# Performance work log

Hardware: AMD Instinct MI355X
Metric: run time of the kernel (lower is better)

The kernel has to match this reference:

```python
import jax, jax.numpy as jnp
import numpy as np

N_QUBITS = 4
DIM = 16  # 2**N_QUBITS
BATCH = 2_097_152


def _pauli_sign_tables():
    # Wire 0 is the most-significant bit in pennylane default.qubit ordering.
    bits = (np.arange(DIM)[:, None] >> np.arange(N_QUBITS - 1, -1, -1)[None, :]) & 1
    z_signs = (1 - 2 * bits).astype(np.float32)  # [16, 4], <Z_i> signs per basis state
    pairs = [(i, j) for i in range(N_QUBITS) for j in range(i + 1, N_QUBITS)]
    zz_signs = np.stack([z_signs[:, i] * z_signs[:, j] for i, j in pairs], axis=1)  # [16, 6]
    return jnp.asarray(z_signs), jnp.asarray(zz_signs)

Z_SIGNS, ZZ_SIGNS = _pauli_sign_tables()


def setup_inputs() -> dict:
    key = jax.random.key(0)
    ks = jax.random.split(key, 6)
    return {
        "x": jax.random.normal(ks[0], (BATCH, DIM), jnp.float32),
        "u_weights": jax.random.normal(ks[1], (N_QUBITS, 2), jnp.float32),
        "w1": jax.random.normal(ks[2], (16, 10), jnp.float32) * 0.3,
        "b1": jnp.zeros((16,), jnp.float32),
        "w2": jax.random.normal(ks[3], (2, 16), jnp.float32) * 0.25,
        "b2": jnp.zeros((2,), jnp.float32),
    }


def _circuit_features(x, u_weights):
    # StatePrep with normalize=True
    state = x / jnp.linalg.norm(x, axis=1, keepdims=True)
    state = state.astype(jnp.complex64).reshape(-1, 2, 2, 2, 2)  # [B, q0, q1, q2, q3]
    half_th = 0.5 * u_weights[:, 0]
    half_ph = 0.5 * u_weights[:, 1]
    c, s = jnp.cos(half_th), jnp.sin(half_th)
    for q in range(N_QUBITS):
        ry = jnp.stack([jnp.stack([c[q], -s[q]]),
                        jnp.stack([s[q], c[q]])]).astype(jnp.complex64)
        e = jnp.exp(-1j * half_ph[q].astype(jnp.complex64))
        rz = jnp.diag(jnp.stack([e, jnp.conj(e)]))
        u = rz @ ry  # RZ(phi) after RY(theta), single fused 2x2 gate
        state = jnp.moveaxis(state, q + 1, -1)
        state = state @ u.T  # new[a] = sum_b u[a,b] * old[b]
        state = jnp.moveaxis(state, -1, q + 1)
    probs = jnp.abs(state.reshape(-1, DIM)) ** 2  # [B, 16]
    z = probs @ Z_SIGNS    # [B, 4]  <Z_i>
    zz = probs @ ZZ_SIGNS  # [B, 6]  <Z_i Z_j>, i<j
    return jnp.concatenate([z, zz], axis=1)  # [B, 10]


def reference(x, u_weights, w1, b1, w2, b2):
    feats = _circuit_features(x, u_weights)
    h = jax.nn.relu(feats @ w1.T + b1)
    return h @ w2.T + b2  # [B, 2]
```

## Files before the change

### kernel.cpp

```cpp
#include <hip/hip_runtime.h>
#include <math.h>


#define PAD 20

__global__ __launch_bounds__(256) void qc_fused(
    const float* __restrict__ x, const float* __restrict__ uw,
    const float* __restrict__ w1, const float* __restrict__ b1,
    const float* __restrict__ w2, const float* __restrict__ b2,
    float* __restrict__ out, long batch)
{
    __shared__ float sX[256 * PAD];
    __shared__ float sCS[8];

    const int t = threadIdx.x;
    if (t < 8) {
        int q = t & 3;
        float th = 0.5f * uw[2 * q];
        sCS[t] = (t < 4) ? cosf(th) : sinf(th);
    }

    const float4* __restrict__ xv4 = (const float4*)x;
    const long nv4 = (long)batch * 4;
    const long base4 = (long)blockIdx.x * 1024;
    if (base4 + 1024 <= nv4) {
#pragma unroll
        for (int r = 0; r < 4; ++r) {
            int f = t + 256 * r;
            float4 v = xv4[base4 + f];
            ((float4*)(sX + (f >> 2) * PAD))[f & 3] = v;
        }
    } else {
#pragma unroll
        for (int r = 0; r < 4; ++r) {
            int f = t + 256 * r;
            long g = base4 + f;
            float4 v = (g < nv4) ? xv4[g] : make_float4(1.f, 0.f, 0.f, 0.f);
            ((float4*)(sX + (f >> 2) * PAD))[f & 3] = v;
        }
    }
    __syncthreads();

    const float* myx = sX + t * PAD;
    float y[16];
#pragma unroll
    for (int i = 0; i < 4; ++i) {
        float4 v = ((const float4*)myx)[i];
        y[4 * i + 0] = v.x; y[4 * i + 1] = v.y;
        y[4 * i + 2] = v.z; y[4 * i + 3] = v.w;
    }

    float cs[4], sn[4];
#pragma unroll
    for (int q = 0; q < 4; ++q) { cs[q] = sCS[q]; sn[q] = sCS[4 + q]; }

#pragma unroll
    for (int q = 0; q < 4; ++q) {
        const int st = 8 >> q;
#pragma unroll
        for (int i = 0; i < 16; ++i) {
            if ((i & st) == 0) {
                float a = y[i], b = y[i + st];
                y[i]      = fmaf(cs[q], a, -sn[q] * b);
                y[i + st] = fmaf(sn[q], a,  cs[q] * b);
            }
        }
    }

    float p[16];
#pragma unroll
    for (int i = 0; i < 16; ++i) p[i] = y[i] * y[i];
#pragma unroll
    for (int st = 1; st < 16; st <<= 1) {
#pragma unroll
        for (int i = 0; i < 16; ++i) {
            if ((i & st) == 0) {
                float a = p[i], b = p[i + st];
                p[i]      = a + b;
                p[i + st] = a - b;
            }
        }
    }

    const float rn = 1.0f / p[0];

    constexpr int bmap[10] = {8, 4, 2, 1, 12, 10, 9, 6, 5, 3};

    float tacc[16];
#pragma unroll
    for (int j = 0; j < 16; ++j) tacc[j] = 0.f;
#pragma unroll
    for (int f = 0; f < 10; ++f) {
        const float pf = p[bmap[f]];
#pragma unroll
        for (int j = 0; j < 16; ++j)
            tacc[j] = fmaf(w1[j * 10 + f], pf, tacc[j]);
    }

    float o0 = b2[0], o1 = b2[1];
#pragma unroll
    for (int j = 0; j < 16; ++j) {
        float h = fmaxf(fmaf(tacc[j], rn, b1[j]), 0.f);
        o0 = fmaf(w2[j],      h, o0);
        o1 = fmaf(w2[16 + j], h, o1);
    }

    const long sidx = (long)blockIdx.x * 256 + t;
    if (sidx < batch) ((float2*)out)[sidx] = make_float2(o0, o1);
}

extern "C" void kernel_launch(void* const* d_in, const int* in_sizes, int n_in,
                              void* d_out, int out_size, void* d_ws, size_t ws_size,
                              hipStream_t stream) {
    const float* x  = (const float*)d_in[0];
    const float* uw = (const float*)d_in[1];
    const float* w1 = (const float*)d_in[2];
    const float* b1 = (const float*)d_in[3];
    const float* w2 = (const float*)d_in[4];
    const float* b2 = (const float*)d_in[5];
    float* out = (float*)d_out;

    long batch = (long)(in_sizes[0] / 16);
    long blocks = (batch + 255) / 256;
    hipLaunchKernelGGL(qc_fused, dim3((unsigned)blocks), dim3(256), 0, stream,
                       x, uw, w1, b1, w2, b2, out, batch);
}
```

Measured before the change: 204.4 us.

## Persistent grid with double-buffered async global-to-LDS loads and XOR swizzle

Turns the kernel into a persistent grid-stride loop capped at 1280 blocks. The next 256-row tile is prefetched into a second LDS buffer with global_load_lds (direct global-to-LDS) while the current tile is computed. Padding is replaced by an XOR swizzle to avoid bank conflicts, and the trig coefficients are computed per thread and made uniform with readfirstlane. The aim is to overlap memory latency with compute on a bandwidth-bound kernel. The costs are a barrier per tile and reliance on builtin async-load semantics (synchronisation relies on __syncthreads waiting on vmcnt). Out-of-range rows now load row 0 instead of a unit vector, though their outputs are never stored.

After: 208.8 us. +2.1%, slower.

```diff
diff --git a/kernel.cpp b/kernel.cpp
--- a/kernel.cpp
+++ b/kernel.cpp
@@ -2,111 +2,124 @@
 #include <math.h>
 
 
-#define PAD 20
+#define TPB 256
 
-__global__ __launch_bounds__(256) void qc_fused(
+__device__ __forceinline__ void async_ld16(const float4* g, float4* l) {
+    __builtin_amdgcn_global_load_lds(
+        (const __attribute__((address_space(1))) void*)g,
+        (__attribute__((address_space(3))) void*)l,
+        16 , 0 , 0 );
+}
+
+__global__ __launch_bounds__(TPB) void qc_fused(
     const float* __restrict__ x, const float* __restrict__ uw,
     const float* __restrict__ w1, const float* __restrict__ b1,
     const float* __restrict__ w2, const float* __restrict__ b2,
     float* __restrict__ out, long batch)
 {
-    __shared__ float sX[256 * PAD];
-    __shared__ float sCS[8];
+    __shared__ float4 sX[2][1024];
 
     const int t = threadIdx.x;
-    if (t < 8) {
-        int q = t & 3;
-        float th = 0.5f * uw[2 * q];
-        sCS[t] = (t < 4) ? cosf(th) : sinf(th);
-    }
-
+    const long ntiles = (batch + TPB - 1) >> 8;
+    const long nv4 = batch * 4;
     const float4* __restrict__ xv4 = (const float4*)x;
-    const long nv4 = (long)batch * 4;
-    const long base4 = (long)blockIdx.x * 1024;
-    if (base4 + 1024 <= nv4) {
-#pragma unroll
-        for (int r = 0; r < 4; ++r) {
-            int f = t + 256 * r;
-            float4 v = xv4[base4 + f];
-            ((float4*)(sX + (f >> 2) * PAD))[f & 3] = v;
-        }
-    } else {
-#pragma unroll
-        for (int r = 0; r < 4; ++r) {
-            int f = t + 256 * r;
-            long g = base4 + f;
-            float4 v = (g < nv4) ? xv4[g] : make_float4(1.f, 0.f, 0.f, 0.f);
-            ((float4*)(sX + (f >> 2) * PAD))[f & 3] = v;
-        }
-    }
-    __syncthreads();
-
-    const float* myx = sX + t * PAD;
-    float y[16];
-#pragma unroll
-    for (int i = 0; i < 4; ++i) {
-        float4 v = ((const float4*)myx)[i];
-        y[4 * i + 0] = v.x; y[4 * i + 1] = v.y;
-        y[4 * i + 2] = v.z; y[4 * i + 3] = v.w;
-    }
 
     float cs[4], sn[4];
 #pragma unroll
-    for (int q = 0; q < 4; ++q) { cs[q] = sCS[q]; sn[q] = sCS[4 + q]; }
+    for (int q = 0; q < 4; ++q) {
+        float th = 0.5f * uw[2 * q];
+        cs[q] = __uint_as_float(__builtin_amdgcn_readfirstlane(__float_as_uint(cosf(th))));
+        sn[q] = __uint_as_float(__builtin_amdgcn_readfirstlane(__float_as_uint(sinf(th))));
+    }
+
+    auto stage = [&](long base4, float4* dst) {
+#pragma unroll
+        for (int r = 0; r < 4; ++r) {
+            int n = (r << 8) + t;
+            int gsw = (n & ~3) | ((n & 3) ^ ((n >> 3) & 3));
+            long g = base4 + gsw;
+            g = (g < nv4) ? g : 0;
+            async_ld16(xv4 + g, dst + n);
+        }
+    };
+
+    long tile = blockIdx.x;
+    int cur = 0;
+    if (tile < ntiles) stage(tile << 10, &sX[0][0]);
+    __syncthreads();
+
+    const int pq = (t >> 1) & 3;
+
+    for (; tile < ntiles; tile += gridDim.x) {
+        const long nxt = tile + gridDim.x;
+        if (nxt < ntiles) stage(nxt << 10, &sX[cur ^ 1][0]);
+
+        const float4* my = &sX[cur][t << 2];
+        float y[16];
+#pragma unroll
+        for (int q = 0; q < 4; ++q) {
+            float4 v = my[q ^ pq];
+            y[4 * q + 0] = v.x; y[4 * q + 1] = v.y;
+            y[4 * q + 2] = v.z; y[4 * q + 3] = v.w;
+        }
 
 #pragma unroll
-    for (int q = 0; q < 4; ++q) {
-        const int st = 8 >> q;
+        for (int q = 0; q < 4; ++q) {
+            const int st = 8 >> q;
 #pragma unroll
-        for (int i = 0; i < 16; ++i) {
-            if ((i & st) == 0) {
-                float a = y[i], b = y[i + st];
-                y[i]      = fmaf(cs[q], a, -sn[q] * b);
-                y[i + st] = fmaf(sn[q], a,  cs[q] * b);
+            for (int i = 0; i < 16; ++i) {
+                if ((i & st) == 0) {
+                    float a = y[i], b = y[i + st];
+                    y[i]      = fmaf(cs[q], a, -sn[q] * b);
+                    y[i + st] = fmaf(sn[q], a,  cs[q] * b);
+                }
             }
         }
-    }
 
-    float p[16];
+        float p[16];
 #pragma unroll
-    for (int i = 0; i < 16; ++i) p[i] = y[i] * y[i];
+        for (int i = 0; i < 16; ++i) p[i] = y[i] * y[i];
 #pragma unroll
-    for (int st = 1; st < 16; st <<= 1) {
+        for (int st = 1; st < 16; st <<= 1) {
 #pragma unroll
-        for (int i = 0; i < 16; ++i) {
-            if ((i & st) == 0) {
-                float a = p[i], b = p[i + st];
-                p[i]      = a + b;
-                p[i + st] = a - b;
+            for (int i = 0; i < 16; ++i) {
+                if ((i & st) == 0) {
+                    float a = p[i], b = p[i + st];
+                    p[i]      = a + b;
+                    p[i + st] = a - b;
+                }
             }
         }
+
+        const float rn = 1.0f / p[0];
+
+        constexpr int bmap[10] = {8, 4, 2, 1, 12, 10, 9, 6, 5, 3};
+
+        float tacc[16];
+#pragma unroll
+        for (int j = 0; j < 16; ++j) tacc[j] = 0.f;
+#pragma unroll
+        for (int f = 0; f < 10; ++f) {
+            const float pf = p[bmap[f]];
+#pragma unroll
+            for (int j = 0; j < 16; ++j)
+                tacc[j] = fmaf(w1[j * 10 + f], pf, tacc[j]);
+        }
+
+        float o0 = b2[0], o1 = b2[1];
+#pragma unroll
+        for (int j = 0; j < 16; ++j) {
+            float h = fmaxf(fmaf(tacc[j], rn, b1[j]), 0.f);
+            o0 = fmaf(w2[j],      h, o0);
+            o1 = fmaf(w2[16 + j], h, o1);
+        }
+
+        const long sidx = (tile << 8) + t;
+        if (sidx < batch) ((float2*)out)[sidx] = make_float2(o0, o1);
+
+        __syncthreads();
+        cur ^= 1;
     }
-
-    const float rn = 1.0f / p[0];
-
-    constexpr int bmap[10] = {8, 4, 2, 1, 12, 10, 9, 6, 5, 3};
-
-    float tacc[16];
-#pragma unroll
-    for (int j = 0; j < 16; ++j) tacc[j] = 0.f;
-#pragma unroll
-    for (int f = 0; f < 10; ++f) {
-        const float pf = p[bmap[f]];
-#pragma unroll
-        for (int j = 0; j < 16; ++j)
-            tacc[j] = fmaf(w1[j * 10 + f], pf, tacc[j]);
-    }
-
-    float o0 = b2[0], o1 = b2[1];
-#pragma unroll
-    for (int j = 0; j < 16; ++j) {
-        float h = fmaxf(fmaf(tacc[j], rn, b1[j]), 0.f);
-        o0 = fmaf(w2[j],      h, o0);
-        o1 = fmaf(w2[16 + j], h, o1);
-    }
-
-    const long sidx = (long)blockIdx.x * 256 + t;
-    if (sidx < batch) ((float2*)out)[sidx] = make_float2(o0, o1);
 }
 
 extern "C" void kernel_launch(void* const* d_in, const int* in_sizes, int n_in,
@@ -121,7 +134,8 @@
     float* out = (float*)d_out;
 
     long batch = (long)(in_sizes[0] / 16);
-    long blocks = (batch + 255) / 256;
+    long ntiles = (batch + 255) / 256;
+    long blocks = ntiles < 1280 ? ntiles : 1280;
     hipLaunchKernelGGL(qc_fused, dim3((unsigned)blocks), dim3(256), 0, stream,
                        x, uw, w1, b1, w2, b2, out, batch);
 }
```
